# Kernel tuning notes

Hardware: AMD Instinct MI355X
Metric: run time of the kernel (lower is better)

Reference implementation:

```python
import jax, jax.numpy as jnp
import numpy as np

H, W, S, B = 256, 256, 16, 8  # dim=(H,W); S hardcoded in forward; B = 1 + events[-1,-1]
N = 4_000_000


def _shift2d(a, dy, dx):
    """Replicates F.pad(a, (pad(dx) + pad(dy)))[:H,:W] where pad(n)=(n,0) if n>=0 else (0,-n).
    Positive diff shifts content right/down and zero-fills; negative diff is a no-op
    (right/bottom padding followed by top-left crop is identity)."""
    sy = jnp.maximum(dy, 0)
    sx = jnp.maximum(dx, 0)
    a = jnp.roll(a, shift=(sy, sx), axis=(0, 1))
    row = jnp.arange(a.shape[0])[:, None]
    col = jnp.arange(a.shape[1])[None, :]
    return jnp.where((row >= sy) & (col >= sx), a, 0.0)


def setup_inputs():
    key = jax.random.key(0)
    k1, k2, k3, k4 = jax.random.split(key, 4)
    x = jax.random.randint(k1, (N,), 0, W).astype(jnp.float32)
    y = jax.random.randint(k2, (N,), 0, H).astype(jnp.float32)
    t = jax.random.uniform(k3, (N,), minval=1e-3, maxval=1.0)
    p = (jax.random.randint(k4, (N,), 0, 2) * 2 - 1).astype(jnp.float32)
    b = jnp.repeat(jnp.arange(B, dtype=jnp.float32), N // B)  # sorted so events[-1,-1]==B-1
    events = jnp.stack([x, y, t, p, b], axis=1)
    return {"events": events}


def _forward(events):
    x = events[:, 0]
    y = events[:, 1]
    t = events[:, 2]
    bi = events[:, 4].astype(jnp.int32)

    # per-batch time normalization: t /= max(t) within each sample
    t_max = jax.ops.segment_max(t, bi, num_segments=B)
    t = t / t_max[bi]

    xi = x.astype(jnp.int32)
    yi = y.astype(jnp.int32)

    # container: per-pixel event count histogram, (B,H,W)
    idx_c = xi + W * yi + W * H * bi
    container = jnp.zeros(B * H * W, jnp.int32).at[idx_c].add(1).reshape(B, H, W)

    # time_segment[e] = number of thresholds i/S (i=1..S-1) with t >= i/S
    thr = jnp.arange(1, S, dtype=t.dtype) / S
    ts = jnp.searchsorted(thr, t, side='right').astype(jnp.int32)

    # combiner accumulates the segment index itself (as in the torch code)
    idx_cb = xi + W * yi + W * H * ts + W * H * S * bi
    combiner = jnp.zeros(B * S * H * W, jnp.int32).at[idx_cb].add(ts)
    combiner = combiner.reshape(B, S, H, W).astype(jnp.float32)

    # per-(batch, segment) event counts and x/y centroids
    seg = bi * S + ts
    cnt = jax.ops.segment_sum(jnp.ones_like(t), seg, num_segments=B * S).reshape(B, S)
    xm = jax.ops.segment_sum(x, seg, num_segments=B * S).reshape(B, S) / cnt
    ym = jax.ops.segment_sum(y, seg, num_segments=B * S).reshape(B, S) / cnt

    # mean-shift alignment + accumulation of the S segment images
    combined = []
    for b_ in range(B):
        segment = combiner[b_, 0]
        x_mean = xm[b_, 0]
        y_mean = ym[b_, 0]
        pts = cnt[b_, 0]  # note: never updated in the original code
        for i in range(1, S):
            cond = cnt[b_, i] > pts
            tmp = jnp.where(cond, segment, combiner[b_, i])
            base = jnp.where(cond, combiner[b_, i], segment)
            dx = jnp.floor(jnp.where(cond, xm[b_, i] - x_mean, x_mean - xm[b_, i])).astype(jnp.int32)
            dy = jnp.floor(jnp.where(cond, ym[b_, i] - y_mean, y_mean - ym[b_, i])).astype(jnp.int32)
            x_mean = jnp.where(cond, xm[b_, i], x_mean)
            y_mean = jnp.where(cond, ym[b_, i], y_mean)
            segment = base + _shift2d(tmp, dy, dx)
        combined.append(jax.nn.relu(segment - S))
    combined_img = jnp.stack(combined)  # (B,H,W)

    # half-resolution count + mean-timestamp voxel grids
    hw4 = (H // 2) * (W // 2)
    idx_ct = xi // 2 + (W // 2) * (yi // 2) + (W * H * bi) // 4
    counter = jnp.zeros(B * hw4, jnp.int32).at[idx_ct].add(1).astype(jnp.float32)
    divider = jnp.where(counter == 0, 1.0, counter)
    timer = jnp.zeros(B * hw4, jnp.float32).at[idx_ct].add(t) / divider
    counter = counter.reshape(B, H // 2, W // 2)
    timer = timer.reshape(B, H // 2, W // 2)

    # 2x2 difference pooling of the count image
    dyv = container[:, ::2] - container[:, 1::2]
    dyv = (dyv[:, :, ::2] + dyv[:, :, 1::2]).astype(jnp.float32)
    dxv = container[:, :, ::2] - container[:, :, 1::2]
    dxv = (dxv[:, 1::2] + dxv[:, ::2]).astype(jnp.float32)

    # F.interpolate(scale_factor=0.5, mode='nearest') == ::2 subsampling for even H,W
    combined_half = combined_img[:, ::2, ::2]

    return jnp.stack([dxv, dyv, timer, counter, combined_half], axis=1)  # (B,5,H/2,W/2)


def reference(events):
    return _forward(events)
```

## Files before the change

### kernel.cpp

```cpp
#include <hip/hip_runtime.h>

#define SS 16
#define BB 8
#define CHUNKS 32

#define OFF_CNT    0
#define OFF_XS     512
#define OFF_YS     1024
#define OFF_BMAX   1536
#define OFF_P4REP  5632
#define OFF_CMREP  (5632 + 16777216)
#define OFF_XYREC  (5632 + 16777216 + 8388608)
#define OFF_TARR   (5632 + 16777216 + 8388608 + 8000000)
#define OFF_TSREC  (5632 + 16777216 + 8388608 + 8000000 + 16000000)


__global__ void k_prep(const float4* __restrict__ ev4, int nq, unsigned* __restrict__ bmax,
                       uint2* __restrict__ xyrec, float4* __restrict__ tarr,
                       int* __restrict__ cnt, int* __restrict__ xs, int* __restrict__ ys) {
    if (blockIdx.x == 0 && threadIdx.x < BB * SS) {
        cnt[threadIdx.x] = 0; xs[threadIdx.x] = 0; ys[threadIdx.x] = 0;
    }
    int bb = blockIdx.x >> 7;
    long base = (long)bb * nq;
    unsigned m = 0;
    for (int q = (blockIdx.x & 127) * blockDim.x + threadIdx.x; q < nq; q += 128 * blockDim.x) {
        const float4* p = ev4 + (base + q) * 5;
        float4 f0 = p[0], f1 = p[1], f2 = p[2], f3 = p[3], f4 = p[4];
        unsigned xy0 = (unsigned)(int)f0.x | ((unsigned)(int)f0.y << 8)
                     | ((unsigned)(int)f1.y << 16) | ((unsigned)(int)f1.z << 24);
        unsigned xy1 = (unsigned)(int)f2.z | ((unsigned)(int)f2.w << 8)
                     | ((unsigned)(int)f3.w << 16) | ((unsigned)(int)f4.x << 24);
        xyrec[base + q] = make_uint2(xy0, xy1);
        tarr[base + q]  = make_float4(f0.z, f1.w, f3.x, f4.y);
        unsigned t0 = __float_as_uint(f0.z), t1 = __float_as_uint(f1.w);
        unsigned t2 = __float_as_uint(f3.x), t3 = __float_as_uint(f4.y);
        unsigned a = t0 > t1 ? t0 : t1;
        unsigned b2 = t2 > t3 ? t2 : t3;
        a = a > b2 ? a : b2;
        m = m > a ? m : a;
    }
    #pragma unroll
    for (int off = 32; off; off >>= 1) {
        unsigned o = (unsigned)__shfl_xor((int)m, off, 64);
        m = m > o ? m : o;
    }
    __shared__ unsigned sm;
    if (threadIdx.x == 0) sm = 0;
    __syncthreads();
    if ((threadIdx.x & 63) == 0) atomicMax(&sm, m);
    __syncthreads();
    if (threadIdx.x == 0) bmax[blockIdx.x] = sm;
}

__global__ void __launch_bounds__(1024, 8)
k_main(const uint2* __restrict__ xyrec, const float4* __restrict__ tarr, int nq,
       const unsigned* __restrict__ bmax,
       unsigned* __restrict__ p4rep, unsigned short* __restrict__ tsrec,
       int* __restrict__ cnt, int* __restrict__ xs, int* __restrict__ ys) {
    __shared__ unsigned p4s[16384];
    __shared__ unsigned long long stat[SS * 8];
    __shared__ unsigned stmax;
    int bb = blockIdx.x >> 5;
    int ch = blockIdx.x & 31;
    if (threadIdx.x == 0) stmax = 0u;
    if (threadIdx.x < SS * 8) stat[threadIdx.x] = 0ull;
    for (int i = threadIdx.x; i < 16384; i += 1024) p4s[i] = 0u;
    __syncthreads();
    if (threadIdx.x < 128) atomicMax(&stmax, bmax[bb * 128 + threadIdx.x]);
    __syncthreads();
    float tm = __uint_as_float(stmax);
    long base = (long)bb * nq;
    int slot = threadIdx.x & 7;
    for (int q = ch * 1024 + threadIdx.x; q < nq; q += CHUNKS * 1024) {
        uint2 xy = xyrec[base + q];
        float4 t4 = tarr[base + q];
        float T[4] = { t4.x, t4.y, t4.z, t4.w };
        unsigned XY[4] = { xy.x & 0xFFFFu, xy.x >> 16, xy.y & 0xFFFFu, xy.y >> 16 };
        unsigned tsn = 0;
        #pragma unroll
        for (int k = 0; k < 4; k++) {
            int xi = (int)(XY[k] & 255u), yi = (int)(XY[k] >> 8);
            float tn = __fdiv_rn(T[k], tm);
            int ts = (int)(tn * 16.0f);
            if (ts > 15) ts = 15;
            unsigned qfix = __float2uint_rn(tn * 256.0f);
            unsigned v = qfix | (1u << 14)
                | (((unsigned)(xi & 1) ^ 1u) << 20)
                | (((unsigned)(yi & 1) ^ 1u) << 26);
            atomicAdd(&p4s[((yi >> 1) << 7) + (xi >> 1)], v);
            atomicAdd(&stat[ts * 8 + slot], 1ull | ((unsigned long long)xi << 20)
                                                 | ((unsigned long long)yi << 42));
            tsn |= (unsigned)ts << (4 * k);
        }
        tsrec[base + q] = (unsigned short)tsn;
    }
    __syncthreads();
    unsigned* dst = p4rep + (long)blockIdx.x * 16384;
    for (int i = threadIdx.x; i < 16384; i += 1024) dst[i] = p4s[i];
    if (threadIdx.x < SS) {
        unsigned long long v = 0ull;
        #pragma unroll
        for (int s = 0; s < 8; s++) v += stat[threadIdx.x * 8 + s];
        if (v) {
            int g = bb * SS + threadIdx.x;
            atomicAdd(&cnt[g], (int)(v & 0xFFFFF));
            atomicAdd(&xs[g],  (int)((v >> 20) & 0x3FFFFF));
            atomicAdd(&ys[g],  (int)(v >> 42));
        }
    }
}

__global__ void __launch_bounds__(1024, 8)
k_comb(const uint2* __restrict__ xyrec, const unsigned short* __restrict__ tsrec, int nq,
       const int* __restrict__ cnt, const int* __restrict__ xs, const int* __restrict__ ys,
       const unsigned* __restrict__ p4rep,
       unsigned* __restrict__ cmrep32, float* __restrict__ out) {
    __shared__ int combs[16384];
    __shared__ double xm[SS], ym[SS];
    __shared__ int cs[SS], ssy[SS], ssx[SS];
    int bb = blockIdx.x >> 5;
    int ch = blockIdx.x & 31;
    for (int i = threadIdx.x; i < 16384; i += 1024) combs[i] = 0;
    if (threadIdx.x < SS) {
        int g = bb * SS + threadIdx.x;
        int cc = cnt[g];
        cs[threadIdx.x] = cc;
        xm[threadIdx.x] = (double)xs[g] / (double)cc;
        ym[threadIdx.x] = (double)ys[g] / (double)cc;
    }
    __syncthreads();
    if (threadIdx.x == 0) {
        double x_mean = xm[0], y_mean = ym[0];
        int c0 = cs[0];
        int sy[SS], sx[SS];
        for (int k = 0; k < SS; k++) { sy[k] = 0; sx[k] = 0; }
        for (int k = 1; k < SS; k++) {
            bool cond = cs[k] > c0;
            double ddx = cond ? (xm[k] - x_mean) : (x_mean - xm[k]);
            double ddy = cond ? (ym[k] - y_mean) : (y_mean - ym[k]);
            int dx = (int)floor(ddx);
            int dy = (int)floor(ddy);
            int px = dx > 0 ? dx : 0;
            int py = dy > 0 ? dy : 0;
            if (cond) {
                for (int j = 0; j < k; j++) { sy[j] += py; sx[j] += px; }
                x_mean = xm[k]; y_mean = ym[k];
            } else {
                sy[k] = py; sx[k] = px;
            }
        }
        for (int k = 0; k < SS; k++) { ssy[k] = sy[k]; ssx[k] = sx[k]; }
    }
    __syncthreads();
    long base = (long)bb * nq;
    for (int q = ch * 1024 + threadIdx.x; q < nq; q += CHUNKS * 1024) {
        uint2 xy = xyrec[base + q];
        unsigned tsn = tsrec[base + q];
        unsigned XY[4] = { xy.x & 0xFFFFu, xy.x >> 16, xy.y & 0xFFFFu, xy.y >> 16 };
        #pragma unroll
        for (int k = 0; k < 4; k++) {
            int ts = (int)((tsn >> (4 * k)) & 15u);
            if (ts) {
                int yy = (int)(XY[k] >> 8) + ssy[ts];
                int xx = (int)(XY[k] & 255u) + ssx[ts];
                if (yy < 256 && xx < 256 && !((yy | xx) & 1))
                    atomicAdd(&combs[((yy >> 1) << 7) + (xx >> 1)], ts);
            }
        }
    }
    __syncthreads();
    unsigned* dst = cmrep32 + (long)blockIdx.x * 8192;
    for (int i = threadIdx.x; i < 8192; i += 1024)
        dst[i] = (unsigned)combs[2 * i] | ((unsigned)combs[2 * i + 1] << 16);
    if (threadIdx.x < 512) {
        int lin = blockIdx.x * 512 + threadIdx.x;
        int hp = lin & 16383;
        int b  = lin >> 14;
        long rb = (long)b * CHUNKS * 16384 + hp;
        unsigned tfix = 0; int c = 0, Ex = 0, Ey = 0;
        #pragma unroll 8
        for (int r = 0; r < CHUNKS; r++) {
            unsigned v = p4rep[rb + (long)r * 16384];
            tfix += v & 0x3FFFu;
            c    += (int)((v >> 14) & 63u);
            Ex   += (int)((v >> 20) & 63u);
            Ey   += (int)(v >> 26);
        }
        float tsum = (float)tfix * (1.0f / 256.0f);
        float ctr = (float)c;
        int obase = (b * 5) << 14;
        out[obase             + hp] = (float)(2 * Ex - c);
        out[obase +     16384 + hp] = (float)(2 * Ey - c);
        out[obase + 2 * 16384 + hp] = tsum / (c == 0 ? 1.0f : ctr);
        out[obase + 3 * 16384 + hp] = ctr;
    }
}

__global__ void k_out(const unsigned short* __restrict__ cmrep,
                      float* __restrict__ out) {
    int lin = blockIdx.x * blockDim.x + threadIdx.x;
    int hp = lin & 16383;
    int b  = lin >> 14;
    long rb = (long)b * CHUNKS * 16384 + hp;
    int cm = 0;
    #pragma unroll 8
    for (int r = 0; r < CHUNKS; r++) cm += cmrep[rb + (long)r * 16384];
    float cmb = (float)cm - 16.0f;
    cmb = cmb < 0.0f ? 0.0f : cmb;
    out[((b * 5 + 4) << 14) + hp] = cmb;
}

extern "C" void kernel_launch(void* const* d_in, const int* in_sizes, int n_in,
                              void* d_out, int out_size, void* d_ws, size_t ws_size,
                              hipStream_t stream) {
    const float4* ev4 = (const float4*)d_in[0];
    int n  = in_sizes[0] / 5;
    int nb = n / BB;
    int nq = nb / 4;
    char* ws = (char*)d_ws;
    int*      cnt   = (int*)     (ws + OFF_CNT);
    int*      xs    = (int*)     (ws + OFF_XS);
    int*      ys    = (int*)     (ws + OFF_YS);
    unsigned* bmax  = (unsigned*)(ws + OFF_BMAX);
    unsigned* p4rep = (unsigned*)(ws + OFF_P4REP);
    unsigned* cmrep32 = (unsigned*)(ws + OFF_CMREP);
    uint2*    xyrec = (uint2*)   (ws + OFF_XYREC);
    float4*   tarr  = (float4*)  (ws + OFF_TARR);
    unsigned short* tsrec = (unsigned short*)(ws + OFF_TSREC);

    hipLaunchKernelGGL(k_prep, dim3(1024), dim3(256),  0, stream, ev4, nq, bmax,
                       xyrec, tarr, cnt, xs, ys);
    hipLaunchKernelGGL(k_main, dim3(256),  dim3(1024), 0, stream, xyrec, tarr, nq,
                       bmax, p4rep, tsrec, cnt, xs, ys);
    hipLaunchKernelGGL(k_comb, dim3(256),  dim3(1024), 0, stream, xyrec, tsrec, nq,
                       cnt, xs, ys, p4rep, cmrep32, (float*)d_out);
    hipLaunchKernelGGL(k_out,  dim3(128),  dim3(1024), 0, stream,
                       (const unsigned short*)cmrep32, (float*)d_out);
}
```

Baseline: 137.4 us.

## Move half-resolution count/time histogram into prep pass using raw timestamps

The shared-memory 2x2 count/parity/timestamp histogram is now built in k_prep, while the raw events are already being read, instead of in k_main. The timestamp is quantized before normalization, and the per-batch max is divided out once per pixel in k_comb. k_prep's grid becomes 256 blocks of 1024 threads so its chunking matches the 32-way replica layout. This lightens k_main's LDS atomic load. In exchange, k_prep holds 64 KB of LDS and does more atomics, and quantizing before normalization changes rounding slightly.

```diff
diff --git a/kernel.cpp b/kernel.cpp
--- a/kernel.cpp
+++ b/kernel.cpp
@@ -15,59 +15,71 @@
 #define OFF_TSREC  (5632 + 16777216 + 8388608 + 8000000 + 16000000)
 
 
-__global__ void k_prep(const float4* __restrict__ ev4, int nq, unsigned* __restrict__ bmax,
-                       uint2* __restrict__ xyrec, float4* __restrict__ tarr,
-                       int* __restrict__ cnt, int* __restrict__ xs, int* __restrict__ ys) {
+__global__ void __launch_bounds__(1024, 8)
+k_prep(const float4* __restrict__ ev4, int nq, unsigned* __restrict__ bmax,
+       uint2* __restrict__ xyrec, float4* __restrict__ tarr,
+       unsigned* __restrict__ p4rep,
+       int* __restrict__ cnt, int* __restrict__ xs, int* __restrict__ ys) {
+    __shared__ unsigned p4s[16384];
+    __shared__ unsigned smax;
     if (blockIdx.x == 0 && threadIdx.x < BB * SS) {
         cnt[threadIdx.x] = 0; xs[threadIdx.x] = 0; ys[threadIdx.x] = 0;
     }
-    int bb = blockIdx.x >> 7;
+    if (threadIdx.x == 0) smax = 0u;
+    for (int i = threadIdx.x; i < 16384; i += 1024) p4s[i] = 0u;
+    __syncthreads();
+    int bb = blockIdx.x >> 5;
+    int ch = blockIdx.x & 31;
     long base = (long)bb * nq;
     unsigned m = 0;
-    for (int q = (blockIdx.x & 127) * blockDim.x + threadIdx.x; q < nq; q += 128 * blockDim.x) {
+    for (int q = ch * 1024 + threadIdx.x; q < nq; q += CHUNKS * 1024) {
         const float4* p = ev4 + (base + q) * 5;
         float4 f0 = p[0], f1 = p[1], f2 = p[2], f3 = p[3], f4 = p[4];
-        unsigned xy0 = (unsigned)(int)f0.x | ((unsigned)(int)f0.y << 8)
-                     | ((unsigned)(int)f1.y << 16) | ((unsigned)(int)f1.z << 24);
-        unsigned xy1 = (unsigned)(int)f2.z | ((unsigned)(int)f2.w << 8)
-                     | ((unsigned)(int)f3.w << 16) | ((unsigned)(int)f4.x << 24);
+        float X[4] = { f0.x, f1.y, f2.z, f3.w };
+        float Y[4] = { f0.y, f1.z, f2.w, f4.x };
+        float T[4] = { f0.z, f1.w, f3.x, f4.y };
+        unsigned xy0 = (unsigned)(int)X[0] | ((unsigned)(int)Y[0] << 8)
+                     | ((unsigned)(int)X[1] << 16) | ((unsigned)(int)Y[1] << 24);
+        unsigned xy1 = (unsigned)(int)X[2] | ((unsigned)(int)Y[2] << 8)
+                     | ((unsigned)(int)X[3] << 16) | ((unsigned)(int)Y[3] << 24);
         xyrec[base + q] = make_uint2(xy0, xy1);
-        tarr[base + q]  = make_float4(f0.z, f1.w, f3.x, f4.y);
-        unsigned t0 = __float_as_uint(f0.z), t1 = __float_as_uint(f1.w);
-        unsigned t2 = __float_as_uint(f3.x), t3 = __float_as_uint(f4.y);
-        unsigned a = t0 > t1 ? t0 : t1;
-        unsigned b2 = t2 > t3 ? t2 : t3;
-        a = a > b2 ? a : b2;
-        m = m > a ? m : a;
+        tarr[base + q]  = make_float4(T[0], T[1], T[2], T[3]);
+        #pragma unroll
+        for (int k = 0; k < 4; k++) {
+            int xi = (int)X[k], yi = (int)Y[k];
+            unsigned t8 = __float2uint_rn(T[k] * 256.0f);
+            unsigned v = t8 | (1u << 14)
+                | (((unsigned)(xi & 1) ^ 1u) << 20)
+                | (((unsigned)(yi & 1) ^ 1u) << 26);
+            atomicAdd(&p4s[((yi >> 1) << 7) + (xi >> 1)], v);
+            unsigned ut = __float_as_uint(T[k]);
+            m = m > ut ? m : ut;
+        }
     }
     #pragma unroll
     for (int off = 32; off; off >>= 1) {
         unsigned o = (unsigned)__shfl_xor((int)m, off, 64);
         m = m > o ? m : o;
     }
-    __shared__ unsigned sm;
-    if (threadIdx.x == 0) sm = 0;
-    __syncthreads();
-    if ((threadIdx.x & 63) == 0) atomicMax(&sm, m);
-    __syncthreads();
-    if (threadIdx.x == 0) bmax[blockIdx.x] = sm;
+    if ((threadIdx.x & 63) == 0) atomicMax(&smax, m);
+    __syncthreads();
+    unsigned* dst = p4rep + (long)blockIdx.x * 16384;
+    for (int i = threadIdx.x; i < 16384; i += 1024) dst[i] = p4s[i];
+    if (threadIdx.x == 0) bmax[blockIdx.x] = smax;
 }
 
 __global__ void __launch_bounds__(1024, 8)
 k_main(const uint2* __restrict__ xyrec, const float4* __restrict__ tarr, int nq,
-       const unsigned* __restrict__ bmax,
-       unsigned* __restrict__ p4rep, unsigned short* __restrict__ tsrec,
+       const unsigned* __restrict__ bmax, unsigned short* __restrict__ tsrec,
        int* __restrict__ cnt, int* __restrict__ xs, int* __restrict__ ys) {
-    __shared__ unsigned p4s[16384];
     __shared__ unsigned long long stat[SS * 8];
     __shared__ unsigned stmax;
     int bb = blockIdx.x >> 5;
     int ch = blockIdx.x & 31;
     if (threadIdx.x == 0) stmax = 0u;
     if (threadIdx.x < SS * 8) stat[threadIdx.x] = 0ull;
-    for (int i = threadIdx.x; i < 16384; i += 1024) p4s[i] = 0u;
-    __syncthreads();
-    if (threadIdx.x < 128) atomicMax(&stmax, bmax[bb * 128 + threadIdx.x]);
+    __syncthreads();
+    if (threadIdx.x < 32) atomicMax(&stmax, bmax[bb * 32 + threadIdx.x]);
     __syncthreads();
     float tm = __uint_as_float(stmax);
     long base = (long)bb * nq;
@@ -84,11 +96,6 @@
             float tn = __fdiv_rn(T[k], tm);
             int ts = (int)(tn * 16.0f);
             if (ts > 15) ts = 15;
-            unsigned qfix = __float2uint_rn(tn * 256.0f);
-            unsigned v = qfix | (1u << 14)
-                | (((unsigned)(xi & 1) ^ 1u) << 20)
-                | (((unsigned)(yi & 1) ^ 1u) << 26);
-            atomicAdd(&p4s[((yi >> 1) << 7) + (xi >> 1)], v);
             atomicAdd(&stat[ts * 8 + slot], 1ull | ((unsigned long long)xi << 20)
                                                  | ((unsigned long long)yi << 42));
             tsn |= (unsigned)ts << (4 * k);
@@ -96,8 +103,6 @@
         tsrec[base + q] = (unsigned short)tsn;
     }
     __syncthreads();
-    unsigned* dst = p4rep + (long)blockIdx.x * 16384;
-    for (int i = threadIdx.x; i < 16384; i += 1024) dst[i] = p4s[i];
     if (threadIdx.x < SS) {
         unsigned long long v = 0ull;
         #pragma unroll
@@ -114,13 +119,15 @@
 __global__ void __launch_bounds__(1024, 8)
 k_comb(const uint2* __restrict__ xyrec, const unsigned short* __restrict__ tsrec, int nq,
        const int* __restrict__ cnt, const int* __restrict__ xs, const int* __restrict__ ys,
-       const unsigned* __restrict__ p4rep,
+       const unsigned* __restrict__ p4rep, const unsigned* __restrict__ bmax,
        unsigned* __restrict__ cmrep32, float* __restrict__ out) {
     __shared__ int combs[16384];
     __shared__ double xm[SS], ym[SS];
     __shared__ int cs[SS], ssy[SS], ssx[SS];
+    __shared__ unsigned stmax;
     int bb = blockIdx.x >> 5;
     int ch = blockIdx.x & 31;
+    if (threadIdx.x == 0) stmax = 0u;
     for (int i = threadIdx.x; i < 16384; i += 1024) combs[i] = 0;
     if (threadIdx.x < SS) {
         int g = bb * SS + threadIdx.x;
@@ -130,6 +137,7 @@
         ym[threadIdx.x] = (double)ys[g] / (double)cc;
     }
     __syncthreads();
+    if (threadIdx.x < 32) atomicMax(&stmax, bmax[bb * 32 + threadIdx.x]);
     if (threadIdx.x == 0) {
         double x_mean = xm[0], y_mean = ym[0];
         int c0 = cs[0];
@@ -174,9 +182,14 @@
     for (int i = threadIdx.x; i < 8192; i += 1024)
         dst[i] = (unsigned)combs[2 * i] | ((unsigned)combs[2 * i + 1] << 16);
     if (threadIdx.x < 512) {
+        float tm = __uint_as_float(stmax);
         int lin = blockIdx.x * 512 + threadIdx.x;
         int hp = lin & 16383;
         int b  = lin >> 14;
+        unsigned bm = 0;
+        #pragma unroll 8
+        for (int i = 0; i < 32; i++) { unsigned v = bmax[b * 32 + i]; bm = bm > v ? bm : v; }
+        tm = __uint_as_float(bm);
         long rb = (long)b * CHUNKS * 16384 + hp;
         unsigned tfix = 0; int c = 0, Ex = 0, Ey = 0;
         #pragma unroll 8
@@ -187,7 +200,7 @@
             Ex   += (int)((v >> 20) & 63u);
             Ey   += (int)(v >> 26);
         }
-        float tsum = (float)tfix * (1.0f / 256.0f);
+        float tsum = (float)tfix * (1.0f / 256.0f) / tm;
         float ctr = (float)c;
         int obase = (b * 5) << 14;
         out[obase             + hp] = (float)(2 * Ex - c);
@@ -229,12 +242,12 @@
     float4*   tarr  = (float4*)  (ws + OFF_TARR);
     unsigned short* tsrec = (unsigned short*)(ws + OFF_TSREC);
 
-    hipLaunchKernelGGL(k_prep, dim3(1024), dim3(256),  0, stream, ev4, nq, bmax,
-                       xyrec, tarr, cnt, xs, ys);
-    hipLaunchKernelGGL(k_main, dim3(256),  dim3(1024), 0, stream, xyrec, tarr, nq,
-                       bmax, p4rep, tsrec, cnt, xs, ys);
-    hipLaunchKernelGGL(k_comb, dim3(256),  dim3(1024), 0, stream, xyrec, tsrec, nq,
-                       cnt, xs, ys, p4rep, cmrep32, (float*)d_out);
-    hipLaunchKernelGGL(k_out,  dim3(128),  dim3(1024), 0, stream,
+    hipLaunchKernelGGL(k_prep, dim3(256), dim3(1024), 0, stream, ev4, nq, bmax,
+                       xyrec, tarr, p4rep, cnt, xs, ys);
+    hipLaunchKernelGGL(k_main, dim3(256), dim3(1024), 0, stream, xyrec, tarr, nq,
+                       bmax, tsrec, cnt, xs, ys);
+    hipLaunchKernelGGL(k_comb, dim3(256), dim3(1024), 0, stream, xyrec, tsrec, nq,
+                       cnt, xs, ys, p4rep, bmax, cmrep32, (float*)d_out);
+    hipLaunchKernelGGL(k_out,  dim3(128), dim3(1024), 0, stream,
                        (const unsigned short*)cmrep32, (float*)d_out);
 }
```

After: 140.5 us. 1.02x slower.
